# Optimization experiments

Measured on AMD Instinct MI355X. Metric: run time of the kernel, lower is better.

The kernel has to match this reference:

```python
import jax, jax.numpy as jnp
import numpy as np

K = 65536          # memory bank size
P = 4096           # partition_size
D = 256            # out_dim
E = 2              # num_experts_per_concept
SMOOTH = 0.1
NUM_TASKS = 1
B = 4096


def setup_inputs() -> dict:
    key = jax.random.key(0)
    k1, k2, k3 = jax.random.split(key, 3)
    queue = jax.random.normal(k1, (D, K), dtype=jnp.float32)
    queue = queue / jnp.linalg.norm(queue, axis=0, keepdims=True)  # normalize(dim=0)
    return {
        "student_embeds": jax.random.normal(k2, (B, D), dtype=jnp.float32),
        "teacher_embeds": jax.random.normal(k3, (B, D), dtype=jnp.float32),
        "queue": queue,
        "student_temp": 0.1,
        "teacher_temp": 0.04,
    }


def _one_task(queue, student_embeds, teacher_embeds, student_temp, teacher_temp, key):
    kperm, ksel = jax.random.split(key)
    # random partition of the bank (torch.randperm + split)
    perm = jax.random.permutation(kperm, K)
    part_idx, mem_idx = perm[:P], perm[P:]
    part = queue[:, part_idx]                      # [D, P]
    mem = queue[:, mem_idx]                        # [D, K-P]
    Kmp = K - P

    sims = part.T @ mem                            # [P, K-P]
    neigh_scores, neigh_idx = jax.lax.top_k(sims, E - 1)  # [P, E-1]

    # append self index (offset into concatenated [mem | part]) and 1-smoothing score
    idx_ = jnp.concatenate([neigh_idx, (Kmp + jnp.arange(P))[:, None]], axis=1)          # [P, E]
    scores_ = jnp.concatenate(
        [neigh_scores, jnp.full((P, 1), 1.0 - SMOOTH, dtype=sims.dtype)], axis=1)        # [P, E]

    # low_energy selection: multinomial(weights, P//2, replacement=False)
    P2 = P // 2
    m = jnp.mean(neigh_scores, axis=-1)            # [P]
    sample_means = jnp.abs(m)
    sample_stds = m                                 # (faithful to source: same quantity)
    coef = (sample_stds / (sample_means + 1e-8)) * (1.0 + 1.0 / (4.0 * Kmp))
    weights = 1.0 / coef                            # [P]
    # Gumbel top-k == multinomial without replacement proportional to weights
    gumbel = jax.random.gumbel(ksel, (P,))
    sel = jax.lax.top_k(jnp.log(weights) + gumbel, P2)[1]   # [P2]
    idx_ = idx_[sel]                                # [P2, E]
    scores_ = scores_[sel]                          # [P2, E]

    embeds_ = jnp.concatenate([mem, part], axis=1)  # [D, K]
    pne = embeds_[:, idx_.reshape(-1)]              # [D, P2*E] partition_neigh_embeddings

    sf = scores_.reshape(-1)                        # [P2*E]
    smooth_val = (1.0 - sf) / (P2 - 1)              # [P2*E]
    # partition_labels = arange(P).repeat_interleave(E)[:P2*E] == repeat(arange(P2), E)
    labels = jnp.repeat(jnp.arange(P2), E)          # [P2*E]
    M = jnp.broadcast_to(smooth_val[:, None], (P2 * E, P2))
    M = M.at[jnp.arange(P2 * E), labels].set(sf)    # scatter_ on dim 1
    M = M / M.sum(-1, keepdims=True)                # row-normalize

    s_probs = jax.nn.softmax(student_embeds @ pne / student_temp, axis=-1) @ M  # [B, P2]
    t_probs = jax.nn.softmax(teacher_embeds @ pne / teacher_temp, axis=-1) @ M  # [B, P2]
    return s_probs, t_probs


def reference(student_embeds, teacher_embeds, queue, student_temp, teacher_temp):
    base = jax.random.key(42)  # internal RNG (torch.randperm / multinomial equivalents)
    s_list, t_list = [], []
    for i in range(NUM_TASKS):
        s, t = _one_task(queue, student_embeds, teacher_embeds,
                         student_temp, teacher_temp, jax.random.fold_in(base, i))
        s_list.append(s)
        t_list.append(t)
    return jnp.stack(s_list), jnp.stack(t_list)  # each [NUM_TASKS, B, P//2]
```

## Files before the change

kernel.cpp:

```cpp
#include <hip/hip_runtime.h>
#include <cstdint>
#include <cmath>
#include <cstring>
#include <vector>
#include <algorithm>
#include <utility>

#define KTOT 65536
#define PP   4096
#define DD   256
#define KMP  61440
#define P2   2048
#define BB   4096
#define NPB  512
#define INVALID_C 0xFFFFFFFFu

static inline void tf2x32(uint32_t k0, uint32_t k1, uint32_t x0, uint32_t x1,
                          uint32_t* o0, uint32_t* o1) {
  static const uint32_t rot[2][4] = {{13u,15u,26u,6u},{17u,29u,16u,24u}};
  uint32_t ks[3] = {k0, k1, 0x1BD11BDAu ^ k0 ^ k1};
  uint32_t v0 = x0 + ks[0], v1 = x1 + ks[1];
  for (int i = 0; i < 5; ++i) {
    const uint32_t* r = rot[i & 1];
    for (int j = 0; j < 4; ++j) {
      v0 += v1;
      v1 = (v1 << r[j]) | (v1 >> (32u - r[j]));
      v1 ^= v0;
    }
    v0 += ks[(i + 1) % 3];
    v1 += ks[(i + 2) % 3] + (uint32_t)(i + 1);
  }
  *o0 = v0; *o1 = v1;
}

static inline uint32_t tf_bits32(uint32_t k0, uint32_t k1, uint32_t i) {
  uint32_t a, b;
  tf2x32(k0, k1, 0u, i, &a, &b);
  return a ^ b;
}

static uint32_t h_mem_idx[KMP];
static uint32_t h_pos_in_mem[KTOT];
static uint32_t h_partsel[P2];

static void host_prepare() {
  uint32_t f0, f1; tf2x32(0u, 42u, 0u, 0u, &f0, &f1);
  uint32_t kperm0, kperm1, ksel0, ksel1;
  tf2x32(f0, f1, 0u, 0u, &kperm0, &kperm1);
  tf2x32(f0, f1, 0u, 1u, &ksel0, &ksel1);

  std::vector<uint32_t> perm(KTOT);
  for (uint32_t i = 0; i < KTOT; ++i) perm[i] = i;
  std::vector<std::pair<uint32_t,uint32_t>> kv(KTOT);
  uint32_t key0 = kperm0, key1 = kperm1;
  for (int round = 0; round < 2; ++round) {
    uint32_t nk0, nk1, sk0, sk1;
    tf2x32(key0, key1, 0u, 0u, &nk0, &nk1);
    tf2x32(key0, key1, 0u, 1u, &sk0, &sk1);
    key0 = nk0; key1 = nk1;
    for (uint32_t i = 0; i < KTOT; ++i) {
      kv[i].first  = tf_bits32(sk0, sk1, i);
      kv[i].second = perm[i];
    }
    std::stable_sort(kv.begin(), kv.end(),
        [](const std::pair<uint32_t,uint32_t>& a,
           const std::pair<uint32_t,uint32_t>& b){ return a.first < b.first; });
    for (uint32_t i = 0; i < KTOT; ++i) perm[i] = kv[i].second;
  }
  static uint32_t part_idx[PP];
  for (int i = 0; i < PP;  ++i) part_idx[i] = perm[i];
  for (int i = 0; i < KMP; ++i) h_mem_idx[i] = perm[PP + i];
  for (int i = 0; i < KTOT; ++i) h_pos_in_mem[i] = INVALID_C;
  for (uint32_t c = 0; c < KMP; ++c) h_pos_in_mem[h_mem_idx[c]] = c;

  static float sval[PP];
  float c1f = (float)(1.0 + 1.0/(4.0*(double)KMP));
  float L0  = logf(1.0f / c1f);
  for (uint32_t i = 0; i < PP; ++i) {
    uint32_t bits = tf_bits32(ksel0, ksel1, i);
    uint32_t fb = (bits >> 9) | 0x3F800000u;
    float f; memcpy(&f, &fb, 4);
    f -= 1.0f;
    float u = (f == 0.0f) ? 1.17549435e-38f : f;
    float g = -logf(-logf(u));
    sval[i] = L0 + g;
  }
  static uint32_t order[PP];
  for (uint32_t i = 0; i < PP; ++i) order[i] = i;
  std::sort(order, order + PP, [](uint32_t a, uint32_t b){
    if (sval[a] != sval[b]) return sval[a] > sval[b];
    return a < b;
  });
  for (int k = 0; k < P2; ++k) h_partsel[k] = part_idx[order[k]];
}

static const bool _host_tables_ready = (host_prepare(), true);

typedef __attribute__((ext_vector_type(8))) short bf16x8;
typedef __attribute__((ext_vector_type(4))) float f32x4;

__device__ inline unsigned short f2bf(float x) {
  union { float f; uint32_t u; } v; v.f = x;
  return (unsigned short)((v.u + 0x7FFFu + ((v.u >> 16) & 1u)) >> 16);
}

__device__ inline void gload16(const unsigned short* g, unsigned short* l) {
  __builtin_amdgcn_global_load_lds(
      (const __attribute__((address_space(1))) unsigned int*)g,
      (__attribute__((address_space(3))) unsigned int*)l, 16, 0, 0);
}

__device__ __host__ inline int swz(int row, int d) {
  return d ^ (((row >> 1) & 3) << 3);
}

__global__ __launch_bounds__(256)
void transpose_bf16(const float* __restrict__ queue, unsigned short* __restrict__ BhT) {
  __shared__ float t[64][65];
  const int tid = threadIdx.x;
  const int c4 = (tid & 15) * 4, r = tid >> 4;
  const int n0 = blockIdx.x * 64, d0 = blockIdx.y * 64;
#pragma unroll
  for (int i = 0; i < 4; ++i) {
    int d = r + i * 16;
    float4 v = *(const float4*)&queue[(d0 + d) * KTOT + n0 + c4];
    t[d][c4 + 0] = v.x; t[d][c4 + 1] = v.y; t[d][c4 + 2] = v.z; t[d][c4 + 3] = v.w;
  }
  __syncthreads();
#pragma unroll
  for (int i = 0; i < 4; ++i) {
    int n = r + i * 16;
    uint32_t lo = (uint32_t)f2bf(t[c4 + 0][n]) | ((uint32_t)f2bf(t[c4 + 1][n]) << 16);
    uint32_t hi = (uint32_t)f2bf(t[c4 + 2][n]) | ((uint32_t)f2bf(t[c4 + 3][n]) << 16);
    uint2 w; w.x = lo; w.y = hi;
    *(uint2*)&BhT[(n0 + n) * DD + swz(n0 + n, d0 + c4)] = w;
  }
}

__global__ __launch_bounds__(256)
void gather_A(const float* __restrict__ queue, const uint32_t* __restrict__ psel,
              float* __restrict__ Apart, unsigned short* __restrict__ AhT) {
  int p = blockIdx.x, d = threadIdx.x;
  float q = queue[d * KTOT + (int)psel[p]];
  Apart[p * DD + d] = q;
  AhT[p * DD + swz(p, d)] = f2bf(q);
}

__global__ __launch_bounds__(256)
void mfma_argmax(const unsigned short* __restrict__ AhT,
                 const unsigned short* __restrict__ BhT,
                 const uint32_t* __restrict__ pos_in_mem,
                 float* __restrict__ pv2, uint32_t* __restrict__ pc2) {
  __shared__ union SM {
    struct { unsigned short As[2][128][32]; unsigned short Bs[2][128][32]; } s;
    struct { float rv[128][33]; uint32_t ri[128][33]; } r;
  } sm;
  const int tid = threadIdx.x;

  const int flat = blockIdx.y * NPB + blockIdx.x;
  const int xcd = flat & 7, job = flat >> 3;
  const int nt = (xcd << 6) + (job >> 4);
  const int mt = job & 15;
  const int m0 = mt * 128, n0 = nt * 128;

  const int wave = tid >> 6, lane = tid & 63;
  const int wm = (wave >> 1) * 64, wn = (wave & 1) * 64;
  const int l15 = lane & 15, quad = lane >> 4;

  f32x4 acc[4][4];
#pragma unroll
  for (int i = 0; i < 4; ++i)
#pragma unroll
    for (int j = 0; j < 4; ++j) acc[i][j] = (f32x4){0.f, 0.f, 0.f, 0.f};

  const int r4 = lane >> 2;
  const int c8 = (lane & 3) * 8;
  const unsigned short* gA0 = &AhT[(m0 + wave * 16 + r4) * DD + c8];
  const unsigned short* gA1 = gA0 + 64 * DD;
  const unsigned short* gB0 = &BhT[(n0 + wave * 16 + r4) * DD + c8];
  const unsigned short* gB1 = gB0 + 64 * DD;

  {
    unsigned short* lA = &sm.s.As[0][wave * 16][0];
    unsigned short* lB = &sm.s.Bs[0][wave * 16][0];
    gload16(gA0, lA); gload16(gA1, lA + 64 * 32);
    gload16(gB0, lB); gload16(gB1, lB + 64 * 32);
  }
  __syncthreads();

  const int swA = ((l15 >> 1) & 3) << 3;
  for (int t = 0; t < 8; ++t) {
    const int cur = t & 1;
    if (t < 7) {
      const int k0 = (t + 1) * 32;
      unsigned short* lA = &sm.s.As[cur ^ 1][wave * 16][0];
      unsigned short* lB = &sm.s.Bs[cur ^ 1][wave * 16][0];
      gload16(gA0 + k0, lA); gload16(gA1 + k0, lA + 64 * 32);
      gload16(gB0 + k0, lB); gload16(gB1 + k0, lB + 64 * 32);
    }
    bf16x8 a[4], b[4];
#pragma unroll
    for (int i = 0; i < 4; ++i)
      a[i] = *(const bf16x8*)&sm.s.As[cur][wm + i * 16 + l15][(quad * 8) ^ swA];
#pragma unroll
    for (int j = 0; j < 4; ++j)
      b[j] = *(const bf16x8*)&sm.s.Bs[cur][wn + j * 16 + l15][(quad * 8) ^ swA];
#pragma unroll
    for (int i = 0; i < 4; ++i)
#pragma unroll
      for (int j = 0; j < 4; ++j)
        acc[i][j] = __builtin_amdgcn_mfma_f32_16x16x32_bf16(a[i], b[j], acc[i][j], 0, 0, 0);
    __syncthreads();
  }

  uint32_t carr[4];
#pragma unroll
  for (int j = 0; j < 4; ++j) carr[j] = pos_in_mem[n0 + wn + j * 16 + l15];
#pragma unroll
  for (int i = 0; i < 4; ++i)
#pragma unroll
    for (int r = 0; r < 4; ++r) {
      float bv = -INFINITY; uint32_t bc = INVALID_C;
#pragma unroll
      for (int j = 0; j < 4; ++j) {
        float v = acc[i][j][r]; uint32_t c = carr[j];
        if (c != INVALID_C && (v > bv || (v == bv && c < bc))) { bv = v; bc = c; }
      }
      int row = wm + i * 16 + quad * 4 + r;
      sm.r.rv[row][(wave & 1) * 16 + l15] = bv;
      sm.r.ri[row][(wave & 1) * 16 + l15] = bc;
    }
  __syncthreads();
  if (tid < 128) {
    float v1 = -INFINITY, v2 = -INFINITY; uint32_t c1 = INVALID_C, c2 = INVALID_C;
#pragma unroll 4
    for (int s = 0; s < 32; ++s) {
      float v = sm.r.rv[tid][s]; uint32_t c = sm.r.ri[tid][s];
      if (c == INVALID_C) continue;
      if (v > v1 || (v == v1 && c < c1)) { v2 = v1; c2 = c1; v1 = v; c1 = c; }
      else if (v > v2 || (v == v2 && c < c2)) { v2 = v; c2 = c; }
    }
    int base = (m0 + tid) * (NPB * 2) + nt * 2;
    pv2[base] = v1;     pc2[base] = c1;
    pv2[base + 1] = v2; pc2[base + 1] = c2;
  }
}

#define EPS_W 0.01f
__global__ __launch_bounds__(256)
void argmax_rescore(const float* __restrict__ pv2, const uint32_t* __restrict__ pc2,
                    const float* __restrict__ Apart, const float* __restrict__ queue,
                    const uint32_t* __restrict__ mem_idx,
                    float* __restrict__ nval, uint32_t* __restrict__ nc) {
  __shared__ float red[256];
  __shared__ uint32_t cand[32];
  __shared__ int cnt;
  const int row = blockIdx.x, tid = threadIdx.x;

  float m = -INFINITY;
  for (int e = tid; e < NPB * 2; e += 256) m = fmaxf(m, pv2[row * (NPB * 2) + e]);
  red[tid] = m; __syncthreads();
  for (int s = 128; s > 0; s >>= 1) {
    if (tid < s) red[tid] = fmaxf(red[tid], red[tid + s]);
    __syncthreads();
  }
  const float M = red[0];
  if (tid == 0) cnt = 0;
  __syncthreads();
  for (int e = tid; e < NPB * 2; e += 256) {
    float v = pv2[row * (NPB * 2) + e]; uint32_t c = pc2[row * (NPB * 2) + e];
    if (c != INVALID_C && v >= M - EPS_W) {
      int k = atomicAdd(&cnt, 1);
      if (k < 32) cand[k] = c;
    }
  }
  __syncthreads();
  const int ncand = min(cnt, 32);
  __shared__ float bestv_s; __shared__ uint32_t bestc_s;
  if (tid == 0) { bestv_s = -INFINITY; bestc_s = INVALID_C; }
  __syncthreads();
  const float av = Apart[row * DD + tid];
  for (int k = 0; k < ncand; ++k) {
    uint32_t c = cand[k];
    int n = (int)mem_idx[c];
    red[tid] = av * queue[tid * KTOT + n];
    __syncthreads();
    for (int s = 128; s > 0; s >>= 1) {
      if (tid < s) red[tid] += red[tid + s];
      __syncthreads();
    }
    if (tid == 0) {
      float sc = red[0];
      if (sc > bestv_s || (sc == bestv_s && c < bestc_s)) { bestv_s = sc; bestc_s = c; }
    }
    __syncthreads();
  }
  if (tid == 0) { nval[row] = bestv_s; nc[row] = bestc_s; }
}

__global__ __launch_bounds__(256)
void prep(const uint32_t* __restrict__ nc, const float* __restrict__ nval,
          const uint32_t* __restrict__ mem_idx, const uint32_t* __restrict__ partsel,
          uint32_t* __restrict__ g_idx, float* __restrict__ svp, float* __restrict__ dp) {
  int k = blockIdx.x * 256 + threadIdx.x;
  if (k >= P2) return;
  uint32_t c = nc[k];
  float sf0 = nval[k];
  float sf1 = 0.9f;
  g_idx[2 * k]     = mem_idx[c];
  g_idx[2 * k + 1] = partsel[k];
  float sv0 = (1.0f - sf0) / 2047.0f;
  float sv1 = (1.0f - sf1) / 2047.0f;
  float rs0 = sf0 + 2047.0f * sv0;
  float rs1 = sf1 + 2047.0f * sv1;
  svp[2 * k]     = sv0 / rs0;  dp[2 * k]     = (sf0 - sv0) / rs0;
  svp[2 * k + 1] = sv1 / rs1;  dp[2 * k + 1] = (sf1 - sv1) / rs1;
}

__global__ __launch_bounds__(256)
void cvt_A(const float* __restrict__ S, const float* __restrict__ T,
           unsigned short* __restrict__ AhS, unsigned short* __restrict__ AlS,
           unsigned short* __restrict__ AhT, unsigned short* __restrict__ AlT) {
  int b = blockIdx.x, d = threadIdx.x;
  const float* src = (b < BB) ? S : T;
  unsigned short* oh = (b < BB) ? AhS : AhT;
  unsigned short* ol = (b < BB) ? AlS : AlT;
  int row = b & (BB - 1);
  float v = src[row * DD + d];
  unsigned short hb = f2bf(v);
  float hf = __uint_as_float((uint32_t)hb << 16);
  unsigned short lb = f2bf(v - hf);
  int o = row * DD + swz(row, d);
  oh[o] = hb;
  ol[o] = lb;
}

__global__ __launch_bounds__(256)
void gather_B(const float* __restrict__ queue, const uint32_t* __restrict__ g_idx,
              unsigned short* __restrict__ Bh, unsigned short* __restrict__ Bl) {
  int r = blockIdx.x, d = threadIdx.x;
  float v = queue[d * KTOT + (int)g_idx[r]];
  unsigned short hb = f2bf(v);
  float hf = __uint_as_float((uint32_t)hb << 16);
  unsigned short lb = f2bf(v - hf);
  int o = r * DD + swz(r, d);
  Bh[o] = hb;
  Bl[o] = lb;
}

__global__ __launch_bounds__(256)
void gemm_split(const unsigned short* __restrict__ Ah,
                const unsigned short* __restrict__ Al,
                const unsigned short* __restrict__ Bh,
                const unsigned short* __restrict__ Bl,
                float* __restrict__ Fo) {
  __shared__ struct { unsigned short As[2][128][32]; unsigned short Bs[2][128][32]; } sm;
  const int tid = threadIdx.x;
  const int m0 = blockIdx.y * 128, n0 = blockIdx.x * 128;
  const int wave = tid >> 6, lane = tid & 63;
  const int wm = (wave >> 1) * 64, wn = (wave & 1) * 64;
  const int l15 = lane & 15, quad = lane >> 4;

  f32x4 acc[4][4];
#pragma unroll
  for (int i = 0; i < 4; ++i)
#pragma unroll
    for (int j = 0; j < 4; ++j) acc[i][j] = (f32x4){0.f, 0.f, 0.f, 0.f};

  const int r4 = lane >> 2;
  const int c8 = (lane & 3) * 8;
  const int aoff = (m0 + wave * 16 + r4) * DD + c8;
  const int boff = (n0 + wave * 16 + r4) * DD + c8;

  {
    unsigned short* lA = &sm.As[0][wave * 16][0];
    unsigned short* lB = &sm.Bs[0][wave * 16][0];
    gload16(Ah + aoff, lA); gload16(Ah + aoff + 64 * DD, lA + 64 * 32);
    gload16(Bh + boff, lB); gload16(Bh + boff + 64 * DD, lB + 64 * 32);
  }
  __syncthreads();

  const int swA = ((l15 >> 1) & 3) << 3;
#pragma unroll 2
  for (int t = 0; t < 24; ++t) {
    const int cur = t & 1;
    if (t < 23) {
      const int tn = t + 1;
      const int p = tn >> 3, k0 = (tn & 7) * 32;
      const unsigned short* ga = ((p == 2) ? Al : Ah) + aoff + k0;
      const unsigned short* gb = ((p == 1) ? Bl : Bh) + boff + k0;
      unsigned short* lA = &sm.As[cur ^ 1][wave * 16][0];
      unsigned short* lB = &sm.Bs[cur ^ 1][wave * 16][0];
      gload16(ga, lA); gload16(ga + 64 * DD, lA + 64 * 32);
      gload16(gb, lB); gload16(gb + 64 * DD, lB + 64 * 32);
    }
    bf16x8 a[4], b[4];
#pragma unroll
    for (int i = 0; i < 4; ++i)
      a[i] = *(const bf16x8*)&sm.As[cur][wm + i * 16 + l15][(quad * 8) ^ swA];
#pragma unroll
    for (int j = 0; j < 4; ++j)
      b[j] = *(const bf16x8*)&sm.Bs[cur][wn + j * 16 + l15][(quad * 8) ^ swA];
#pragma unroll
    for (int i = 0; i < 4; ++i)
#pragma unroll
      for (int j = 0; j < 4; ++j)
        acc[i][j] = __builtin_amdgcn_mfma_f32_16x16x32_bf16(a[i], b[j], acc[i][j], 0, 0, 0);
    __syncthreads();
  }

#pragma unroll
  for (int i = 0; i < 4; ++i)
#pragma unroll
    for (int j = 0; j < 4; ++j)
#pragma unroll
      for (int r = 0; r < 4; ++r)
        Fo[(m0 + wm + i * 16 + quad * 4 + r) * PP + n0 + wn + j * 16 + l15] = acc[i][j][r];
}

__global__ __launch_bounds__(256)
void softmax_out(const float* __restrict__ F, const float* __restrict__ temp_ptr,
                 const float* __restrict__ svp, const float* __restrict__ dp,
                 float* __restrict__ out) {
  __shared__ float e[PP];
  __shared__ float red[256];
  int b = blockIdx.x, tid = threadIdx.x;
  float temp = temp_ptr[0];
  float lmax = -INFINITY;
  for (int r = tid; r < PP; r += 256) {
    float l = F[b * PP + r] / temp;
    e[r] = l;
    lmax = fmaxf(lmax, l);
  }
  red[tid] = lmax; __syncthreads();
  for (int s = 128; s > 0; s >>= 1) {
    if (tid < s) red[tid] = fmaxf(red[tid], red[tid + s]);
    __syncthreads();
  }
  lmax = red[0]; __syncthreads();

  float z = 0.0f, sacc = 0.0f;
  for (int r = tid; r < PP; r += 256) {
    float ev = expf(e[r] - lmax);
    e[r] = ev;
    z += ev;
    sacc = fmaf(ev, svp[r], sacc);
  }
  red[tid] = z; __syncthreads();
  for (int s = 128; s > 0; s >>= 1) {
    if (tid < s) red[tid] += red[tid + s];
    __syncthreads();
  }
  z = red[0]; __syncthreads();
  red[tid] = sacc; __syncthreads();
  for (int s = 128; s > 0; s >>= 1) {
    if (tid < s) red[tid] += red[tid + s];
    __syncthreads();
  }
  sacc = red[0]; __syncthreads();

  float invz = 1.0f / z;
  for (int j = tid; j < P2; j += 256) {
    float v = sacc + e[2 * j] * dp[2 * j] + e[2 * j + 1] * dp[2 * j + 1];
    out[b * P2 + j] = v * invz;
  }
}

#define OFF_BHT      0u
#define OFF_PV2      33554432u
#define OFF_PC2      41943040u
#define OFF_AHT      50331648u
#define OFF_APART    51380224u
#define OFF_F        0u
#define OFF_BH       33554432u
#define OFF_BL       35651584u
#define OFF_AHS      37748736u
#define OFF_ALS      39845888u
#define OFF_AHT2     41943040u
#define OFF_ALT2     44040192u
#define OFF_SVP      71303168u
#define OFF_DP       71319552u
#define OFF_GIDX     71335936u
#define OFF_NVAL     71352320u
#define OFF_NC       71360512u
#define OFF_UP_MEM   71368704u
#define OFF_UP_POS   71614464u
#define OFF_UP_PSEL  71876608u

extern "C" void kernel_launch(void* const* d_in, const int* in_sizes, int n_in,
                              void* d_out, int out_size, void* d_ws, size_t ws_size,
                              hipStream_t stream) {
  (void)in_sizes; (void)n_in; (void)out_size; (void)ws_size;
  (void)_host_tables_ready;
  const float* d_student = (const float*)d_in[0];
  const float* d_teacher = (const float*)d_in[1];
  const float* d_queue   = (const float*)d_in[2];
  const float* d_stemp   = (const float*)d_in[3];
  const float* d_ttemp   = (const float*)d_in[4];
  float* out = (float*)d_out;
  char* ws = (char*)d_ws;

  unsigned short* BhT   = (unsigned short*)(ws + OFF_BHT);
  float*          pv2   = (float*)(ws + OFF_PV2);
  uint32_t*       pc2   = (uint32_t*)(ws + OFF_PC2);
  unsigned short* AhT   = (unsigned short*)(ws + OFF_AHT);
  float*          Apart = (float*)(ws + OFF_APART);
  float*          F     = (float*)(ws + OFF_F);
  unsigned short* Bh    = (unsigned short*)(ws + OFF_BH);
  unsigned short* Bl    = (unsigned short*)(ws + OFF_BL);
  unsigned short* AhS   = (unsigned short*)(ws + OFF_AHS);
  unsigned short* AlS   = (unsigned short*)(ws + OFF_ALS);
  unsigned short* AhT2  = (unsigned short*)(ws + OFF_AHT2);
  unsigned short* AlT2  = (unsigned short*)(ws + OFF_ALT2);
  float*          svp   = (float*)(ws + OFF_SVP);
  float*          dp    = (float*)(ws + OFF_DP);
  uint32_t*       g_idx = (uint32_t*)(ws + OFF_GIDX);
  float*          nval  = (float*)(ws + OFF_NVAL);
  uint32_t*       nc    = (uint32_t*)(ws + OFF_NC);
  uint32_t*       dMemIdx = (uint32_t*)(ws + OFF_UP_MEM);
  uint32_t*       dPosMem = (uint32_t*)(ws + OFF_UP_POS);
  uint32_t*       dPSel   = (uint32_t*)(ws + OFF_UP_PSEL);

  hipMemcpyAsync(dMemIdx, h_mem_idx,    KMP  * sizeof(uint32_t), hipMemcpyHostToDevice, stream);
  hipMemcpyAsync(dPosMem, h_pos_in_mem, KTOT * sizeof(uint32_t), hipMemcpyHostToDevice, stream);
  hipMemcpyAsync(dPSel,   h_partsel,    P2   * sizeof(uint32_t), hipMemcpyHostToDevice, stream);

  transpose_bf16<<<dim3(KTOT / 64, DD / 64), 256, 0, stream>>>(d_queue, BhT);
  gather_A<<<P2, 256, 0, stream>>>(d_queue, dPSel, Apart, AhT);
  mfma_argmax<<<dim3(NPB, P2 / 128), 256, 0, stream>>>(AhT, BhT, dPosMem, pv2, pc2);
  argmax_rescore<<<P2, 256, 0, stream>>>(pv2, pc2, Apart, d_queue, dMemIdx, nval, nc);
  prep<<<P2 / 256, 256, 0, stream>>>(nc, nval, dMemIdx, dPSel, g_idx, svp, dp);

  cvt_A<<<2 * BB, 256, 0, stream>>>(d_student, d_teacher, AhS, AlS, AhT2, AlT2);
  gather_B<<<PP, 256, 0, stream>>>(d_queue, g_idx, Bh, Bl);

  for (int half = 0; half < 2; ++half) {
    gemm_split<<<dim3(PP / 128, 2048 / 128), 256, 0, stream>>>(
        AhS + (size_t)half * 2048 * DD, AlS + (size_t)half * 2048 * DD, Bh, Bl, F);
    softmax_out<<<2048, 256, 0, stream>>>(F, d_stemp, svp, dp,
        out + (size_t)half * 2048 * P2);
  }
  for (int half = 0; half < 2; ++half) {
    gemm_split<<<dim3(PP / 128, 2048 / 128), 256, 0, stream>>>(
        AhT2 + (size_t)half * 2048 * DD, AlT2 + (size_t)half * 2048 * DD, Bh, Bl, F);
    softmax_out<<<2048, 256, 0, stream>>>(F, d_ttemp, svp, dp,
        out + (size_t)BB * P2 + (size_t)half * 2048 * P2);
  }
}
```

Baseline: 578.4 us.

## Make mfma_argmax blocks loop over eight N tiles with continuous pipelining

```diff
diff --git a/kernel.cpp b/kernel.cpp
--- a/kernel.cpp
+++ b/kernel.cpp
@@ -151,17 +151,20 @@
                  const unsigned short* __restrict__ BhT,
                  const uint32_t* __restrict__ pos_in_mem,
                  float* __restrict__ pv2, uint32_t* __restrict__ pc2) {
-  __shared__ union SM {
-    struct { unsigned short As[2][128][32]; unsigned short Bs[2][128][32]; } s;
-    struct { float rv[128][33]; uint32_t ri[128][33]; } r;
+  __shared__ struct {
+    unsigned short As[2][128][32];
+    unsigned short Bs[2][128][32];
+    float rv[128][33];
+    uint32_t ri[128][33];
   } sm;
   const int tid = threadIdx.x;
 
-  const int flat = blockIdx.y * NPB + blockIdx.x;
+  const int flat = blockIdx.x;
   const int xcd = flat & 7, job = flat >> 3;
-  const int nt = (xcd << 6) + (job >> 4);
+  const int ng = (xcd << 3) + (job >> 4);
   const int mt = job & 15;
-  const int m0 = mt * 128, n0 = nt * 128;
+  const int m0 = mt * 128;
+  const int nbase = ng * 8;
 
   const int wave = tid >> 6, lane = tid & 63;
   const int wm = (wave >> 1) * 64, wn = (wave & 1) * 64;
@@ -177,72 +180,120 @@
   const int c8 = (lane & 3) * 8;
   const unsigned short* gA0 = &AhT[(m0 + wave * 16 + r4) * DD + c8];
   const unsigned short* gA1 = gA0 + 64 * DD;
-  const unsigned short* gB0 = &BhT[(n0 + wave * 16 + r4) * DD + c8];
+  const unsigned short* gB0 = &BhT[(nbase * 128 + wave * 16 + r4) * DD + c8];
   const unsigned short* gB1 = gB0 + 64 * DD;
 
   {
-    unsigned short* lA = &sm.s.As[0][wave * 16][0];
-    unsigned short* lB = &sm.s.Bs[0][wave * 16][0];
+    unsigned short* lA = &sm.As[0][wave * 16][0];
+    unsigned short* lB = &sm.Bs[0][wave * 16][0];
     gload16(gA0, lA); gload16(gA1, lA + 64 * 32);
     gload16(gB0, lB); gload16(gB1, lB + 64 * 32);
   }
   __syncthreads();
 
   const int swA = ((l15 >> 1) & 3) << 3;
-  for (int t = 0; t < 8; ++t) {
-    const int cur = t & 1;
-    if (t < 7) {
-      const int k0 = (t + 1) * 32;
-      unsigned short* lA = &sm.s.As[cur ^ 1][wave * 16][0];
-      unsigned short* lB = &sm.s.Bs[cur ^ 1][wave * 16][0];
-      gload16(gA0 + k0, lA); gload16(gA1 + k0, lA + 64 * 32);
-      gload16(gB0 + k0, lB); gload16(gB1 + k0, lB + 64 * 32);
-    }
-    bf16x8 a[4], b[4];
+
+  for (int g = 0; g < 8; ++g) {
+    const int gstep = g * (128 * DD);
+#pragma unroll
+    for (int k = 0; k < 8; ++k) {
+      const int T = g * 8 + k;
+      const int cur = T & 1;
+      if (k < 7 || g < 7) {
+        const int kn = ((k + 1) & 7) * 32;
+        const int gs = (k < 7) ? gstep : gstep + 128 * DD;
+        unsigned short* lA = &sm.As[cur ^ 1][wave * 16][0];
+        unsigned short* lB = &sm.Bs[cur ^ 1][wave * 16][0];
+        gload16(gA0 + kn, lA); gload16(gA1 + kn, lA + 64 * 32);
+        gload16(gB0 + gs + kn, lB); gload16(gB1 + gs + kn, lB + 64 * 32);
+      }
+      if (k == 0 && g > 0) {
+        const int n0e = (nbase + g - 1) * 128;
+        uint32_t carr[4];
+#pragma unroll
+        for (int j = 0; j < 4; ++j) carr[j] = pos_in_mem[n0e + wn + j * 16 + l15];
+#pragma unroll
+        for (int i = 0; i < 4; ++i)
+#pragma unroll
+          for (int r = 0; r < 4; ++r) {
+            float bv = -INFINITY; uint32_t bc = INVALID_C;
+#pragma unroll
+            for (int j = 0; j < 4; ++j) {
+              float v = acc[i][j][r]; uint32_t c = carr[j];
+              if (c != INVALID_C && (v > bv || (v == bv && c < bc))) { bv = v; bc = c; }
+            }
+            int row = wm + i * 16 + quad * 4 + r;
+            sm.rv[row][(wave & 1) * 16 + l15] = bv;
+            sm.ri[row][(wave & 1) * 16 + l15] = bc;
+          }
+        __syncthreads();
+        if (tid < 128) {
+          float v1 = -INFINITY, v2 = -INFINITY; uint32_t c1 = INVALID_C, c2 = INVALID_C;
+#pragma unroll 4
+          for (int s = 0; s < 32; ++s) {
+            float v = sm.rv[tid][s]; uint32_t c = sm.ri[tid][s];
+            if (c == INVALID_C) continue;
+            if (v > v1 || (v == v1 && c < c1)) { v2 = v1; c2 = c1; v1 = v; c1 = c; }
+            else if (v > v2 || (v == v2 && c < c2)) { v2 = v; c2 = c; }
+          }
+          int base = (m0 + tid) * (NPB * 2) + (nbase + g - 1) * 2;
+          pv2[base] = v1;     pc2[base] = c1;
+          pv2[base + 1] = v2; pc2[base + 1] = c2;
+        }
+#pragma unroll
+        for (int i = 0; i < 4; ++i)
+#pragma unroll
+          for (int j = 0; j < 4; ++j) acc[i][j] = (f32x4){0.f, 0.f, 0.f, 0.f};
+      }
+      bf16x8 a[4], b[4];
+#pragma unroll
+      for (int i = 0; i < 4; ++i)
+        a[i] = *(const bf16x8*)&sm.As[cur][wm + i * 16 + l15][(quad * 8) ^ swA];
+#pragma unroll
+      for (int j = 0; j < 4; ++j)
+        b[j] = *(const bf16x8*)&sm.Bs[cur][wn + j * 16 + l15][(quad * 8) ^ swA];
+#pragma unroll
+      for (int i = 0; i < 4; ++i)
+#pragma unroll
+        for (int j = 0; j < 4; ++j)
+          acc[i][j] = __builtin_amdgcn_mfma_f32_16x16x32_bf16(a[i], b[j], acc[i][j], 0, 0, 0);
+      __syncthreads();
+    }
+  }
+
+  {
+    const int n0e = (nbase + 7) * 128;
+    uint32_t carr[4];
+#pragma unroll
+    for (int j = 0; j < 4; ++j) carr[j] = pos_in_mem[n0e + wn + j * 16 + l15];
 #pragma unroll
     for (int i = 0; i < 4; ++i)
-      a[i] = *(const bf16x8*)&sm.s.As[cur][wm + i * 16 + l15][(quad * 8) ^ swA];
-#pragma unroll
-    for (int j = 0; j < 4; ++j)
-      b[j] = *(const bf16x8*)&sm.s.Bs[cur][wn + j * 16 + l15][(quad * 8) ^ swA];
-#pragma unroll
-    for (int i = 0; i < 4; ++i)
-#pragma unroll
-      for (int j = 0; j < 4; ++j)
-        acc[i][j] = __builtin_amdgcn_mfma_f32_16x16x32_bf16(a[i], b[j], acc[i][j], 0, 0, 0);
-    __syncthreads();
-  }
-
-  uint32_t carr[4];
-#pragma unroll
-  for (int j = 0; j < 4; ++j) carr[j] = pos_in_mem[n0 + wn + j * 16 + l15];
-#pragma unroll
-  for (int i = 0; i < 4; ++i)
-#pragma unroll
-    for (int r = 0; r < 4; ++r) {
-      float bv = -INFINITY; uint32_t bc = INVALID_C;
-#pragma unroll
-      for (int j = 0; j < 4; ++j) {
-        float v = acc[i][j][r]; uint32_t c = carr[j];
-        if (c != INVALID_C && (v > bv || (v == bv && c < bc))) { bv = v; bc = c; }
+#pragma unroll
+      for (int r = 0; r < 4; ++r) {
+        float bv = -INFINITY; uint32_t bc = INVALID_C;
+#pragma unroll
+        for (int j = 0; j < 4; ++j) {
+          float v = acc[i][j][r]; uint32_t c = carr[j];
+          if (c != INVALID_C && (v > bv || (v == bv && c < bc))) { bv = v; bc = c; }
+        }
+        int row = wm + i * 16 + quad * 4 + r;
+        sm.rv[row][(wave & 1) * 16 + l15] = bv;
+        sm.ri[row][(wave & 1) * 16 + l15] = bc;
       }
-      int row = wm + i * 16 + quad * 4 + r;
-      sm.r.rv[row][(wave & 1) * 16 + l15] = bv;
-      sm.r.ri[row][(wave & 1) * 16 + l15] = bc;
-    }
-  __syncthreads();
-  if (tid < 128) {
-    float v1 = -INFINITY, v2 = -INFINITY; uint32_t c1 = INVALID_C, c2 = INVALID_C;
+    __syncthreads();
+    if (tid < 128) {
+      float v1 = -INFINITY, v2 = -INFINITY; uint32_t c1 = INVALID_C, c2 = INVALID_C;
 #pragma unroll 4
-    for (int s = 0; s < 32; ++s) {
-      float v = sm.r.rv[tid][s]; uint32_t c = sm.r.ri[tid][s];
-      if (c == INVALID_C) continue;
-      if (v > v1 || (v == v1 && c < c1)) { v2 = v1; c2 = c1; v1 = v; c1 = c; }
-      else if (v > v2 || (v == v2 && c < c2)) { v2 = v; c2 = c; }
-    }
-    int base = (m0 + tid) * (NPB * 2) + nt * 2;
-    pv2[base] = v1;     pc2[base] = c1;
-    pv2[base + 1] = v2; pc2[base + 1] = c2;
+      for (int s = 0; s < 32; ++s) {
+        float v = sm.rv[tid][s]; uint32_t c = sm.ri[tid][s];
+        if (c == INVALID_C) continue;
+        if (v > v1 || (v == v1 && c < c1)) { v2 = v1; c2 = c1; v1 = v; c1 = c; }
+        else if (v > v2 || (v == v2 && c < c2)) { v2 = v; c2 = c; }
+      }
+      int base = (m0 + tid) * (NPB * 2) + (nbase + 7) * 2;
+      pv2[base] = v1;     pc2[base] = c1;
+      pv2[base + 1] = v2; pc2[base + 1] = c2;
+    }
   }
 }
 
@@ -527,7 +578,7 @@
 
   transpose_bf16<<<dim3(KTOT / 64, DD / 64), 256, 0, stream>>>(d_queue, BhT);
   gather_A<<<P2, 256, 0, stream>>>(d_queue, dPSel, Apart, AhT);
-  mfma_argmax<<<dim3(NPB, P2 / 128), 256, 0, stream>>>(AhT, BhT, dPosMem, pv2, pc2);
+  mfma_argmax<<<1024, 256, 0, stream>>>(AhT, BhT, dPosMem, pv2, pc2);
   argmax_rescore<<<P2, 256, 0, stream>>>(pv2, pc2, Apart, d_queue, dMemIdx, nval, nc);
   prep<<<P2 / 256, 256, 0, stream>>>(nc, nval, dMemIdx, dPSel, g_idx, svp, dp);
 
```

New measurement: 801.4 us. 38.6% more time.

## Triple-buffer LDS staging in MFMA GEMM kernels with explicit vmcnt waits

Applied to the files above, without the earlier changes.

```diff
diff --git a/kernel.cpp b/kernel.cpp
--- a/kernel.cpp
+++ b/kernel.cpp
@@ -152,7 +152,7 @@
                  const uint32_t* __restrict__ pos_in_mem,
                  float* __restrict__ pv2, uint32_t* __restrict__ pc2) {
   __shared__ union SM {
-    struct { unsigned short As[2][128][32]; unsigned short Bs[2][128][32]; } s;
+    struct { unsigned short As[3][128][32]; unsigned short Bs[3][128][32]; } s;
     struct { float rv[128][33]; uint32_t ri[128][33]; } r;
   } sm;
   const int tid = threadIdx.x;
@@ -180,24 +180,24 @@
   const unsigned short* gB0 = &BhT[(n0 + wave * 16 + r4) * DD + c8];
   const unsigned short* gB1 = gB0 + 64 * DD;
 
-  {
-    unsigned short* lA = &sm.s.As[0][wave * 16][0];
-    unsigned short* lB = &sm.s.Bs[0][wave * 16][0];
-    gload16(gA0, lA); gload16(gA1, lA + 64 * 32);
-    gload16(gB0, lB); gload16(gB1, lB + 64 * 32);
-  }
-  __syncthreads();
+  auto STAGE = [&](int buf, int kt) {
+    unsigned short* lA = &sm.s.As[buf][wave * 16][0];
+    unsigned short* lB = &sm.s.Bs[buf][wave * 16][0];
+    const int k0 = kt * 32;
+    gload16(gA0 + k0, lA); gload16(gA1 + k0, lA + 64 * 32);
+    gload16(gB0 + k0, lB); gload16(gB1 + k0, lB + 64 * 32);
+  };
+
+  STAGE(0, 0); STAGE(1, 1); STAGE(2, 2);
+  asm volatile("s_waitcnt vmcnt(8)" ::: "memory");
+  __builtin_amdgcn_sched_barrier(0);
+  __builtin_amdgcn_s_barrier();
+  __builtin_amdgcn_sched_barrier(0);
 
   const int swA = ((l15 >> 1) & 3) << 3;
+#pragma unroll
   for (int t = 0; t < 8; ++t) {
-    const int cur = t & 1;
-    if (t < 7) {
-      const int k0 = (t + 1) * 32;
-      unsigned short* lA = &sm.s.As[cur ^ 1][wave * 16][0];
-      unsigned short* lB = &sm.s.Bs[cur ^ 1][wave * 16][0];
-      gload16(gA0 + k0, lA); gload16(gA1 + k0, lA + 64 * 32);
-      gload16(gB0 + k0, lB); gload16(gB1 + k0, lB + 64 * 32);
-    }
+    const int cur = t % 3;
     bf16x8 a[4], b[4];
 #pragma unroll
     for (int i = 0; i < 4; ++i)
@@ -205,12 +205,24 @@
 #pragma unroll
     for (int j = 0; j < 4; ++j)
       b[j] = *(const bf16x8*)&sm.s.Bs[cur][wn + j * 16 + l15][(quad * 8) ^ swA];
+    asm volatile("s_waitcnt lgkmcnt(0)" ::: "memory");
+    __builtin_amdgcn_sched_barrier(0);
+    __builtin_amdgcn_s_barrier();
+    __builtin_amdgcn_sched_barrier(0);
+    if (t + 3 < 8) STAGE(cur, t + 3);
 #pragma unroll
     for (int i = 0; i < 4; ++i)
 #pragma unroll
       for (int j = 0; j < 4; ++j)
         acc[i][j] = __builtin_amdgcn_mfma_f32_16x16x32_bf16(a[i], b[j], acc[i][j], 0, 0, 0);
-    __syncthreads();
+    if (t < 7) {
+      if (t < 5)       asm volatile("s_waitcnt vmcnt(8)" ::: "memory");
+      else if (t == 5) asm volatile("s_waitcnt vmcnt(4)" ::: "memory");
+      else             asm volatile("s_waitcnt vmcnt(0)" ::: "memory");
+      __builtin_amdgcn_sched_barrier(0);
+      __builtin_amdgcn_s_barrier();
+      __builtin_amdgcn_sched_barrier(0);
+    }
   }
 
   uint32_t carr[4];
@@ -354,7 +366,7 @@
                 const unsigned short* __restrict__ Bh,
                 const unsigned short* __restrict__ Bl,
                 float* __restrict__ Fo) {
-  __shared__ struct { unsigned short As[2][128][32]; unsigned short Bs[2][128][32]; } sm;
+  __shared__ struct { unsigned short As[3][128][32]; unsigned short Bs[3][128][32]; } sm;
   const int tid = threadIdx.x;
   const int m0 = blockIdx.y * 128, n0 = blockIdx.x * 128;
   const int wave = tid >> 6, lane = tid & 63;
@@ -372,28 +384,26 @@
   const int aoff = (m0 + wave * 16 + r4) * DD + c8;
   const int boff = (n0 + wave * 16 + r4) * DD + c8;
 
-  {
-    unsigned short* lA = &sm.As[0][wave * 16][0];
-    unsigned short* lB = &sm.Bs[0][wave * 16][0];
-    gload16(Ah + aoff, lA); gload16(Ah + aoff + 64 * DD, lA + 64 * 32);
-    gload16(Bh + boff, lB); gload16(Bh + boff + 64 * DD, lB + 64 * 32);
-  }
-  __syncthreads();
+  auto STAGE = [&](int buf, int tt) {
+    const int p = tt >> 3, k0 = (tt & 7) * 32;
+    const unsigned short* ga = ((p == 2) ? Al : Ah) + aoff + k0;
+    const unsigned short* gb = ((p == 1) ? Bl : Bh) + boff + k0;
+    unsigned short* lA = &sm.As[buf][wave * 16][0];
+    unsigned short* lB = &sm.Bs[buf][wave * 16][0];
+    gload16(ga, lA); gload16(ga + 64 * DD, lA + 64 * 32);
+    gload16(gb, lB); gload16(gb + 64 * DD, lB + 64 * 32);
+  };
+
+  STAGE(0, 0); STAGE(1, 1); STAGE(2, 2);
+  asm volatile("s_waitcnt vmcnt(8)" ::: "memory");
+  __builtin_amdgcn_sched_barrier(0);
+  __builtin_amdgcn_s_barrier();
+  __builtin_amdgcn_sched_barrier(0);
 
   const int swA = ((l15 >> 1) & 3) << 3;
-#pragma unroll 2
+#pragma unroll
   for (int t = 0; t < 24; ++t) {
-    const int cur = t & 1;
-    if (t < 23) {
-      const int tn = t + 1;
-      const int p = tn >> 3, k0 = (tn & 7) * 32;
-      const unsigned short* ga = ((p == 2) ? Al : Ah) + aoff + k0;
-      const unsigned short* gb = ((p == 1) ? Bl : Bh) + boff + k0;
-      unsigned short* lA = &sm.As[cur ^ 1][wave * 16][0];
-      unsigned short* lB = &sm.Bs[cur ^ 1][wave * 16][0];
-      gload16(ga, lA); gload16(ga + 64 * DD, lA + 64 * 32);
-      gload16(gb, lB); gload16(gb + 64 * DD, lB + 64 * 32);
-    }
+    const int cur = t % 3;
     bf16x8 a[4], b[4];
 #pragma unroll
     for (int i = 0; i < 4; ++i)
@@ -401,12 +411,24 @@
 #pragma unroll
     for (int j = 0; j < 4; ++j)
       b[j] = *(const bf16x8*)&sm.Bs[cur][wn + j * 16 + l15][(quad * 8) ^ swA];
+    asm volatile("s_waitcnt lgkmcnt(0)" ::: "memory");
+    __builtin_amdgcn_sched_barrier(0);
+    __builtin_amdgcn_s_barrier();
+    __builtin_amdgcn_sched_barrier(0);
+    if (t + 3 < 24) STAGE(cur, t + 3);
 #pragma unroll
     for (int i = 0; i < 4; ++i)
 #pragma unroll
       for (int j = 0; j < 4; ++j)
         acc[i][j] = __builtin_amdgcn_mfma_f32_16x16x32_bf16(a[i], b[j], acc[i][j], 0, 0, 0);
-    __syncthreads();
+    if (t < 23) {
+      if (t <= 20)      asm volatile("s_waitcnt vmcnt(8)" ::: "memory");
+      else if (t == 21) asm volatile("s_waitcnt vmcnt(4)" ::: "memory");
+      else              asm volatile("s_waitcnt vmcnt(0)" ::: "memory");
+      __builtin_amdgcn_sched_barrier(0);
+      __builtin_amdgcn_s_barrier();
+      __builtin_amdgcn_sched_barrier(0);
+    }
   }
 
 #pragma unroll
```

Measured after the change: 626.0 us. 8.2% more time.
